# Optimization experiments

Hardware: AMD Instinct MI355X
Metric: run time of the kernel (lower is better)

## Reference

```python
import jax, jax.numpy as jnp
import numpy as np

D_MODEL = 96
N_HEAD = 3
HEAD_DIM = D_MODEL // N_HEAD  # 32
D_FF = 2048
WIDTH = 65
HALF_W = (WIDTH - 1) // 2  # 32
EPS = 1e-5


def layer_norm(x, g, b):
    mu = jnp.mean(x, axis=-1, keepdims=True)
    var = jnp.mean(jnp.square(x - mu), axis=-1, keepdims=True)
    return (x - mu) * jax.lax.rsqrt(var + EPS) * g + b


def setup_inputs() -> dict:
    key = jax.random.key(0)
    ks = jax.random.split(key, 8)
    B, T = 8, 2048
    s = 0.05
    return {
        "x": jax.random.normal(ks[0], (B, D_MODEL, T), dtype=jnp.float32),
        "w_qkv": jax.random.normal(ks[1], (3 * D_MODEL, D_MODEL), dtype=jnp.float32) * s,
        "b_qkv": jnp.zeros((3 * D_MODEL,), dtype=jnp.float32),
        "w_out": jax.random.normal(ks[2], (D_MODEL, D_MODEL), dtype=jnp.float32) * s,
        "b_out": jnp.zeros((D_MODEL,), dtype=jnp.float32),
        "ln1_g": jnp.ones((D_MODEL,), dtype=jnp.float32),
        "ln1_b": jnp.zeros((D_MODEL,), dtype=jnp.float32),
        "w_ff1": jax.random.normal(ks[3], (D_FF, D_MODEL), dtype=jnp.float32) * s,
        "b_ff1": jnp.zeros((D_FF,), dtype=jnp.float32),
        "w_ff2": jax.random.normal(ks[4], (D_MODEL, D_FF), dtype=jnp.float32) * s,
        "b_ff2": jnp.zeros((D_MODEL,), dtype=jnp.float32),
        "ln2_g": jnp.ones((D_MODEL,), dtype=jnp.float32),
        "ln2_b": jnp.zeros((D_MODEL,), dtype=jnp.float32),
        "lnf_g": jnp.ones((D_MODEL,), dtype=jnp.float32),
        "lnf_b": jnp.zeros((D_MODEL,), dtype=jnp.float32),
    }


def reference(x, w_qkv, b_qkv, w_out, b_out, ln1_g, ln1_b, w_ff1, b_ff1,
              w_ff2, b_ff2, ln2_g, ln2_b, lnf_g, lnf_b):
    # x: (B, C, T) -> (B, T, C)
    h = jnp.transpose(x, (0, 2, 1))
    B, T, C = h.shape

    # --- multi-head self-attention with banded mask ---
    qkv = h @ w_qkv.T + b_qkv                      # (B, T, 3C)
    q, k, v = jnp.split(qkv, 3, axis=-1)
    q = q.reshape(B, T, N_HEAD, HEAD_DIM)
    k = k.reshape(B, T, N_HEAD, HEAD_DIM)
    v = v.reshape(B, T, N_HEAD, HEAD_DIM)

    scale = 1.0 / jnp.sqrt(jnp.float32(HEAD_DIM))
    scores = jnp.einsum("bthd,bshd->bhts", q, k) * scale  # (B, H, T, T)

    idx = jnp.arange(T)
    band = jnp.abs(idx[:, None] - idx[None, :]) <= HALF_W  # |i-j| <= half width
    scores = jnp.where(band[None, None], scores, jnp.float32(-jnp.inf))

    attn = jax.nn.softmax(scores, axis=-1)
    ctx = jnp.einsum("bhts,bshd->bthd", attn, v).reshape(B, T, C)
    attn_out = ctx @ w_out.T + b_out

    # --- post-norm encoder layer (dropout inactive / eval mode) ---
    h = layer_norm(h + attn_out, ln1_g, ln1_b)
    ff = jax.nn.relu(h @ w_ff1.T + b_ff1) @ w_ff2.T + b_ff2
    h = layer_norm(h + ff, ln2_g, ln2_b)

    # extra layernorm applied when width is not None
    h = layer_norm(h, lnf_g, lnf_b)

    # (B, T, C) -> (B, C, T)
    return jnp.transpose(h, (0, 2, 1))
```

## Files before the change

kernel.cpp:

```cpp
#include <hip/hip_runtime.h>
#include <hip/hip_bf16.h>

#define B 8
#define T 2048
#define C 96
#define NH 3
#define HD 32
#define FFD 2048
#define HALF_W 32
#define BT (B*T)

typedef __hip_bfloat16 bf16;
typedef __attribute__((ext_vector_type(8))) short short8;
typedef __attribute__((ext_vector_type(4))) short short4v;
typedef __attribute__((ext_vector_type(16))) float floatx16;

__device__ __forceinline__ short f2bs(float v){
    __hip_bfloat16 h = __float2bfloat16(v);
    return *reinterpret_cast<short*>(&h);
}
__device__ __forceinline__ int imin(int a, int b){ return a < b ? a : b; }
__device__ __forceinline__ int imax(int a, int b){ return a > b ? a : b; }
__device__ __forceinline__ short8 ld_b64x2(const short* p){
    short4v a = *(const short4v*)p;
    short4v b = *(const short4v*)(p + 4);
    short8 v;
    v[0]=a[0]; v[1]=a[1]; v[2]=a[2]; v[3]=a[3];
    v[4]=b[0]; v[5]=b[1]; v[6]=b[2]; v[7]=b[3];
    return v;
}

__global__ void cvtw_kernel(const float* __restrict__ wq, const float* __restrict__ wo,
                            const float* __restrict__ w1, const float* __restrict__ w2,
                            bf16* __restrict__ dst){
    int i = blockIdx.x*256 + threadIdx.x;
    if(i < 27648)       dst[i] = __float2bfloat16(wq[i]);
    else if(i < 36864)  dst[i] = __float2bfloat16(wo[i-27648]);
    else if(i < 233472) dst[i] = __float2bfloat16(w1[i-36864]);
    else if(i < 430080) dst[i] = __float2bfloat16(w2[i-233472]);
}

__global__ __launch_bounds__(256) void qkv_kernel(
    const float* __restrict__ x, const bf16* __restrict__ wq,
    const float* __restrict__ bias, bf16* __restrict__ qkvs){
    __shared__ float xs[96*36];
    int b  = blockIdx.x >> 6;
    int t0 = (blockIdx.x & 63) * 32;
    for(int e = threadIdx.x; e < 96*8; e += 256){
        int c = e >> 3, t4 = e & 7;
        *(float4*)(xs + c*36 + t4*4) =
            *(const float4*)(x + (size_t)b*C*T + (size_t)c*T + t0 + t4*4);
    }
    __syncthreads();
    int r0 = b*T + t0;
    const int w = threadIdx.x >> 6, lane = threadIdx.x & 63;
    const int lm = lane & 31, hq = lane >> 5;
    short8 bfr[6];
    #pragma unroll
    for(int ks = 0; ks < 6; ++ks){
        short8 v;
        #pragma unroll
        for(int i = 0; i < 8; ++i)
            v[i] = f2bs(xs[(ks*16 + hq*8 + i)*36 + lm]);
        bfr[ks] = v;
    }
    int nacc = (w == 0) ? 3 : 2;
    int ots[3] = {w, w+4, 8};
    floatx16 acc[3];
    #pragma unroll
    for(int i = 0; i < 3; ++i)
        #pragma unroll
        for(int r = 0; r < 16; ++r) acc[i][r] = 0.f;
    #pragma unroll
    for(int i = 0; i < 3; ++i){
        if(i < nacc){
            #pragma unroll
            for(int ks = 0; ks < 6; ++ks){
                short8 af = *(const short8*)((const short*)wq
                              + (size_t)(ots[i]*32 + lm)*96 + ks*16 + hq*8);
                acc[i] = __builtin_amdgcn_mfma_f32_32x32x16_bf16(af, bfr[ks], acc[i], 0,0,0);
            }
        }
    }
    #pragma unroll
    for(int i = 0; i < 3; ++i){
        if(i < nacc){
            int type = ots[i]/3, hh = ots[i]%3;
            size_t rowbase = (((size_t)type*B*NH) + (size_t)b*NH + hh)*T + t0 + lm;
            #pragma unroll
            for(int q = 0; q < 4; ++q){
                float4 bv = *(const float4*)(bias + ots[i]*32 + 8*q + 4*hq);
                short4v pk;
                pk[0] = f2bs(acc[i][4*q+0] + bv.x);
                pk[1] = f2bs(acc[i][4*q+1] + bv.y);
                pk[2] = f2bs(acc[i][4*q+2] + bv.z);
                pk[3] = f2bs(acc[i][4*q+3] + bv.w);
                *(short4v*)((short*)qkvs + rowbase*32 + 8*q + 4*hq) = pk;
            }
        }
    }
}

__global__ __launch_bounds__(128) void attn_kernel(const bf16* __restrict__ qkvs,
                                                   bf16* __restrict__ ctxh){
    __shared__ __align__(16) short VtS[32*132];
    __shared__ __align__(16) short PtS[2][32*100];
    __shared__ float LsS[2][32];
    int blk = blockIdx.x;
    int ntile = T/64;
    int b   = blk / (NH*ntile);
    int rem = blk % (NH*ntile);
    int h   = rem / ntile;
    int t0  = (rem % ntile) * 64;
    const short* qb = (const short*)qkvs + ((size_t)0*B*NH + (size_t)b*NH + h)*T*32;
    const short* kb = (const short*)qkvs + ((size_t)1*B*NH + (size_t)b*NH + h)*T*32;
    const short* vb = (const short*)qkvs + ((size_t)2*B*NH + (size_t)b*NH + h)*T*32;
    const int tid = threadIdx.x;
    const int w = tid >> 6, lane = tid & 63;
    const int lm = lane & 31, hq = lane >> 5;

    for(int e = tid; e < 256; e += 128){
        int kp = e >> 2, d8 = e & 3;
        int sa = imin(imax(t0 - 32 + 2*kp, 0), T-1);
        int sb = imin(imax(t0 - 32 + 2*kp + 1, 0), T-1);
        short8 va = *(const short8*)(vb + (size_t)sa*32 + d8*8);
        short8 v2 = *(const short8*)(vb + (size_t)sb*32 + d8*8);
        #pragma unroll
        for(int j = 0; j < 8; ++j){
            int val = (int)(unsigned short)va[j] | ((int)(unsigned short)v2[j] << 16);
            *(int*)(VtS + (d8*8 + j)*132 + 2*kp) = val;
        }
    }
    short8 qf0, qf1;
    {
        const short* qrow = qb + (size_t)(t0 + 32*w + lm)*32;
        qf0 = *(const short8*)(qrow + hq*8);
        qf1 = *(const short8*)(qrow + 16 + hq*8);
    }
    floatx16 S[3];
    #pragma unroll
    for(int sub = 0; sub < 3; ++sub){
        int srow = imin(imax(t0 + 32*w - 32 + sub*32 + lm, 0), T-1);
        const short* krow = kb + (size_t)srow*32;
        short8 kf0 = *(const short8*)(krow + hq*8);
        short8 kf1 = *(const short8*)(krow + 16 + hq*8);
        floatx16 z;
        #pragma unroll
        for(int r = 0; r < 16; ++r) z[r] = 0.f;
        z = __builtin_amdgcn_mfma_f32_32x32x16_bf16(kf0, qf0, z, 0,0,0);
        z = __builtin_amdgcn_mfma_f32_32x32x16_bf16(kf1, qf1, z, 0,0,0);
        S[sub] = z;
    }
    const float scale = 0.17677669529663687f;
    float part = 0.f;
    #pragma unroll
    for(int sub = 0; sub < 3; ++sub){
        #pragma unroll
        for(int r = 0; r < 16; ++r){
            int key_local = sub*32 + (r&3) + 8*(r>>2) + 4*hq;
            int s_glob = t0 + 32*w - 32 + key_local;
            int rel = key_local - lm;
            bool ok = (rel >= 0) && (rel <= 64) && (s_glob >= 0) && (s_glob < T);
            float p = ok ? __expf(S[sub][r]*scale) : 0.f;
            S[sub][r] = p;
            part += p;
        }
    }
    float ltot = part + __shfl_xor(part, 32);
    if(hq == 0) LsS[w][lm] = ltot;
    #pragma unroll
    for(int sub = 0; sub < 3; ++sub){
        #pragma unroll
        for(int q4 = 0; q4 < 4; ++q4){
            int kbase = sub*32 + 8*q4 + 4*hq;
            short4v pk;
            pk[0] = f2bs(S[sub][4*q4+0]);
            pk[1] = f2bs(S[sub][4*q4+1]);
            pk[2] = f2bs(S[sub][4*q4+2]);
            pk[3] = f2bs(S[sub][4*q4+3]);
            *(short4v*)(PtS[w] + lm*100 + kbase) = pk;
        }
    }
    __syncthreads();
    floatx16 O;
    #pragma unroll
    for(int r = 0; r < 16; ++r) O[r] = 0.f;
    #pragma unroll
    for(int ks = 0; ks < 6; ++ks){
        short8 pa = ld_b64x2(PtS[w] + lm*100 + ks*16 + hq*8);
        short8 vf = ld_b64x2(VtS + lm*132 + 32*w + ks*16 + hq*8);
        O = __builtin_amdgcn_mfma_f32_32x32x16_bf16(pa, vf, O, 0,0,0);
    }
    #pragma unroll
    for(int r = 0; r < 16; ++r){
        int qr = (r&3) + 8*(r>>2) + 4*hq;
        float linv = 1.f / LsS[w][qr];
        ((short*)ctxh)[(((size_t)b*NH + h)*T + t0 + 32*w + qr)*32 + lm] = f2bs(O[r]*linv);
    }
}

__global__ __launch_bounds__(192) void outproj_ln_kernel(
    const bf16* __restrict__ ctxh, const bf16* __restrict__ wo,
    const float* __restrict__ bias, const float* __restrict__ x,
    const float* __restrict__ g1, const float* __restrict__ bb1,
    float* __restrict__ h1, bf16* __restrict__ h1b){
    __shared__ float red[2][3][32];
    const int ct = threadIdx.x >> 6, lane = threadIdx.x & 63;
    const int lm = lane & 31, hq = lane >> 5;
    const int r0 = blockIdx.x * 32;
    const int b = r0 / T, tloc = r0 % T;
    short8 bfr[6];
    #pragma unroll
    for(int ks = 0; ks < 6; ++ks){
        int off = ks*16 + hq*8;
        int hh = off >> 5, dd = off & 31;
        bfr[ks] = *(const short8*)((const short*)ctxh
                    + (((size_t)b*NH + hh)*T + tloc + lm)*32 + dd);
    }
    floatx16 acc;
    #pragma unroll
    for(int r = 0; r < 16; ++r) acc[r] = 0.f;
    #pragma unroll
    for(int ks = 0; ks < 6; ++ks){
        short8 af = *(const short8*)((const short*)wo
                      + (size_t)(ct*32 + lm)*96 + ks*16 + hq*8);
        acc = __builtin_amdgcn_mfma_f32_32x32x16_bf16(af, bfr[ks], acc, 0,0,0);
    }
    float vals[16];
    float p1 = 0.f, p2 = 0.f;
    #pragma unroll
    for(int q = 0; q < 4; ++q){
        int c = ct*32 + 8*q + 4*hq;
        float4 bv = *(const float4*)(bias + c);
        float bva[4] = {bv.x, bv.y, bv.z, bv.w};
        #pragma unroll
        for(int r = 0; r < 4; ++r){
            float xv = x[(size_t)b*C*T + (size_t)(c + r)*T + tloc + lm];
            float v = acc[4*q+r] + bva[r] + xv;
            vals[4*q+r] = v;
            p1 += v; p2 += v*v;
        }
    }
    p1 += __shfl_xor(p1, 32);
    p2 += __shfl_xor(p2, 32);
    if(hq == 0){ red[0][ct][lm] = p1; red[1][ct][lm] = p2; }
    __syncthreads();
    float s  = red[0][0][lm] + red[0][1][lm] + red[0][2][lm];
    float s2 = red[1][0][lm] + red[1][1][lm] + red[1][2][lm];
    float mu = s * (1.0f/96.0f);
    float rstd = rsqrtf(s2*(1.0f/96.0f) - mu*mu + 1e-5f);
    int row = r0 + lm;
    #pragma unroll
    for(int q = 0; q < 4; ++q){
        int c = ct*32 + 8*q + 4*hq;
        float4 gv = *(const float4*)(g1 + c);
        float4 bv = *(const float4*)(bb1 + c);
        float ga[4] = {gv.x, gv.y, gv.z, gv.w};
        float ba[4] = {bv.x, bv.y, bv.z, bv.w};
        float4 yo;
        float ya[4];
        #pragma unroll
        for(int r = 0; r < 4; ++r)
            ya[r] = (vals[4*q+r] - mu)*rstd*ga[r] + ba[r];
        yo.x = ya[0]; yo.y = ya[1]; yo.z = ya[2]; yo.w = ya[3];
        *(float4*)(h1 + (size_t)row*96 + c) = yo;
        short4v pk;
        #pragma unroll
        for(int r = 0; r < 4; ++r) pk[r] = f2bs(ya[r]);
        *(short4v*)((short*)h1b + (size_t)row*96 + c) = pk;
    }
}

__global__ __launch_bounds__(256) void ff_ln_kernel(
    const bf16* __restrict__ h1b, const float* __restrict__ h1,
    const bf16* __restrict__ w1b, const float* __restrict__ b1,
    const bf16* __restrict__ w2b, const float* __restrict__ b2,
    const float* __restrict__ g2, const float* __restrict__ bt2,
    const float* __restrict__ gf, const float* __restrict__ btf,
    float* __restrict__ out){
    __shared__ __align__(16) short sst[32*132];
    __shared__ float redp[9*1088];
    __shared__ float zt[96*33];
    const int tid = threadIdx.x;
    const int w = tid >> 6, lane = tid & 63;
    const int lm = lane & 31, hq = lane >> 5;
    const int r0 = blockIdx.x * 32;
    short8 hf[6];
    #pragma unroll
    for(int ks = 0; ks < 6; ++ks)
        hf[ks] = *(const short8*)((const short*)h1b
                   + (size_t)(r0 + lm)*96 + ks*16 + hq*8);
    floatx16 acc2[3];
    #pragma unroll
    for(int i = 0; i < 3; ++i)
        #pragma unroll
        for(int r = 0; r < 16; ++r) acc2[i][r] = 0.f;
    for(int jt = 0; jt < 16; ++jt){
        const int j0 = jt * 128;
        floatx16 a0;
        #pragma unroll
        for(int r = 0; r < 16; ++r) a0[r] = 0.f;
        #pragma unroll
        for(int ks = 0; ks < 6; ++ks){
            short8 af = *(const short8*)((const short*)w1b
                          + (size_t)(j0 + w*32 + lm)*96 + ks*16 + hq*8);
            a0 = __builtin_amdgcn_mfma_f32_32x32x16_bf16(af, hf[ks], a0, 0,0,0);
        }
        #pragma unroll
        for(int q = 0; q < 4; ++q){
            float4 bv = *(const float4*)(b1 + j0 + w*32 + 8*q + 4*hq);
            float bva[4] = {bv.x, bv.y, bv.z, bv.w};
            short4v pk;
            #pragma unroll
            for(int r = 0; r < 4; ++r){
                float v = a0[4*q+r] + bva[r];
                pk[r] = f2bs(v > 0.f ? v : 0.f);
            }
            *(short4v*)(sst + lm*132 + w*32 + 8*q + 4*hq) = pk;
        }
        #pragma unroll
        for(int g = 0; g < 2; ++g){
            int jl0 = w*32 + g*16;
            short8 sf = ld_b64x2(sst + lm*132 + jl0 + hq*8);
            #pragma unroll
            for(int ct = 0; ct < 3; ++ct){
                short8 wf = *(const short8*)((const short*)w2b
                              + (size_t)(ct*32 + lm)*FFD + j0 + jl0 + hq*8);
                acc2[ct] = __builtin_amdgcn_mfma_f32_32x32x16_bf16(wf, sf, acc2[ct], 0,0,0);
            }
        }
    }
    __syncthreads();
    if(w > 0){
        #pragma unroll
        for(int ct = 0; ct < 3; ++ct)
            #pragma unroll
            for(int q = 0; q < 4; ++q)
                #pragma unroll
                for(int r = 0; r < 4; ++r)
                    redp[((w-1)*3 + ct)*1088 + lane*17 + 4*q + r] = acc2[ct][4*q+r];
    }
    __syncthreads();
    if(w == 0){
        float vals[48];
        float p1 = 0.f, p2 = 0.f;
        #pragma unroll
        for(int ct = 0; ct < 3; ++ct){
            #pragma unroll
            for(int q = 0; q < 4; ++q){
                int c = ct*32 + 8*q + 4*hq;
                float4 bv = *(const float4*)(b2 + c);
                float4 rs = *(const float4*)(h1 + (size_t)(r0 + lm)*96 + c);
                float bva[4] = {bv.x, bv.y, bv.z, bv.w};
                float rsa[4] = {rs.x, rs.y, rs.z, rs.w};
                #pragma unroll
                for(int r = 0; r < 4; ++r){
                    float v = acc2[ct][4*q+r]
                            + redp[(0*3 + ct)*1088 + lane*17 + 4*q + r]
                            + redp[(1*3 + ct)*1088 + lane*17 + 4*q + r]
                            + redp[(2*3 + ct)*1088 + lane*17 + 4*q + r]
                            + bva[r] + rsa[r];
                    vals[ct*16 + 4*q + r] = v;
                    p1 += v; p2 += v*v;
                }
            }
        }
        p1 += __shfl_xor(p1, 32);
        p2 += __shfl_xor(p2, 32);
        float mu = p1*(1.0f/96.0f);
        float rstd = rsqrtf(p2*(1.0f/96.0f) - mu*mu + 1e-5f);
        float q1 = 0.f, q2 = 0.f;
        #pragma unroll
        for(int ct = 0; ct < 3; ++ct){
            #pragma unroll
            for(int q = 0; q < 4; ++q){
                int c = ct*32 + 8*q + 4*hq;
                float4 gv = *(const float4*)(g2 + c);
                float4 bv = *(const float4*)(bt2 + c);
                float ga[4] = {gv.x, gv.y, gv.z, gv.w};
                float ba[4] = {bv.x, bv.y, bv.z, bv.w};
                #pragma unroll
                for(int r = 0; r < 4; ++r){
                    float y = (vals[ct*16+4*q+r] - mu)*rstd*ga[r] + ba[r];
                    vals[ct*16+4*q+r] = y;
                    q1 += y; q2 += y*y;
                }
            }
        }
        q1 += __shfl_xor(q1, 32);
        q2 += __shfl_xor(q2, 32);
        float mu2 = q1*(1.0f/96.0f);
        float rstd2 = rsqrtf(q2*(1.0f/96.0f) - mu2*mu2 + 1e-5f);
        #pragma unroll
        for(int ct = 0; ct < 3; ++ct){
            #pragma unroll
            for(int q = 0; q < 4; ++q){
                int c = ct*32 + 8*q + 4*hq;
                float4 gv = *(const float4*)(gf + c);
                float4 bv = *(const float4*)(btf + c);
                float ga[4] = {gv.x, gv.y, gv.z, gv.w};
                float ba[4] = {bv.x, bv.y, bv.z, bv.w};
                #pragma unroll
                for(int r = 0; r < 4; ++r)
                    zt[(c + r)*33 + lm] = (vals[ct*16+4*q+r] - mu2)*rstd2*ga[r] + ba[r];
            }
        }
    }
    __syncthreads();
    int bb  = r0 / T;
    int t0g = r0 % T;
    for(int e = tid; e < 96*32; e += 256){
        int c = e >> 5, tt = e & 31;
        out[(size_t)bb*C*T + (size_t)c*T + t0g + tt] = zt[c*33 + tt];
    }
}

extern "C" void kernel_launch(void* const* d_in, const int* in_sizes, int n_in,
                              void* d_out, int out_size, void* d_ws, size_t ws_size,
                              hipStream_t stream) {
    const float* x     = (const float*)d_in[0];
    const float* w_qkv = (const float*)d_in[1];
    const float* b_qkv = (const float*)d_in[2];
    const float* w_out = (const float*)d_in[3];
    const float* b_out = (const float*)d_in[4];
    const float* ln1_g = (const float*)d_in[5];
    const float* ln1_b = (const float*)d_in[6];
    const float* w_ff1 = (const float*)d_in[7];
    const float* b_ff1 = (const float*)d_in[8];
    const float* w_ff2 = (const float*)d_in[9];
    const float* b_ff2 = (const float*)d_in[10];
    const float* ln2_g = (const float*)d_in[11];
    const float* ln2_b = (const float*)d_in[12];
    const float* lnf_g = (const float*)d_in[13];
    const float* lnf_b = (const float*)d_in[14];
    float* out = (float*)d_out;

    char* wsb = (char*)d_ws;
    bf16*  qkvs  = (bf16*)wsb;
    bf16*  ctxh  = (bf16*)(wsb + 9437184);
    float* h1    = (float*)(wsb + 12582912);
    bf16*  h1b   = (bf16*)(wsb + 18874368);
    bf16*  wts   = (bf16*)(wsb + 22020096);
    bf16*  wqkvb = wts;
    bf16*  woutb = wts + 27648;
    bf16*  w1b   = wts + 36864;
    bf16*  w2b   = wts + 233472;

    cvtw_kernel      <<<1680, 256, 0, stream>>>(w_qkv, w_out, w_ff1, w_ff2, wts);
    qkv_kernel       <<<BT/32, 256, 0, stream>>>(x, wqkvb, b_qkv, qkvs);
    attn_kernel      <<<B*NH*(T/64), 128, 0, stream>>>(qkvs, ctxh);
    outproj_ln_kernel<<<BT/32, 192, 0, stream>>>(ctxh, woutb, b_out, x,
                                                 ln1_g, ln1_b, h1, h1b);
    ff_ln_kernel     <<<BT/32, 256, 0, stream>>>(h1b, h1, w1b, b_ff1, w2b, b_ff2,
                                                 ln2_g, ln2_b, lnf_g, lnf_b, out);
}
```

Baseline: 151.8 us.

## Prefetch FF weights, split MFMA chains, and pass FF1 output via lane shuffles

Restructures the FF inner loop. W1 fragments for the next tile are prefetched into registers, and the W2 fragments are loaded at the start of each iteration. The FF1 MFMA chain is split into two independent accumulators to shorten the dependency chain. The shared-memory staging of the ReLU output is replaced with cross-half-wave shuffles, and the loop is fully unrolled with occupancy hinted at two blocks. This targets global-load latency and LDS round trips, at the cost of higher register pressure, which may cause spills under the new launch bound.

```diff
diff --git a/kernel.cpp b/kernel.cpp
--- a/kernel.cpp
+++ b/kernel.cpp
@@ -271,14 +271,13 @@
     }
 }
 
-__global__ __launch_bounds__(256) void ff_ln_kernel(
+__global__ __launch_bounds__(256, 2) void ff_ln_kernel(
     const bf16* __restrict__ h1b, const float* __restrict__ h1,
     const bf16* __restrict__ w1b, const float* __restrict__ b1,
     const bf16* __restrict__ w2b, const float* __restrict__ b2,
     const float* __restrict__ g2, const float* __restrict__ bt2,
     const float* __restrict__ gf, const float* __restrict__ btf,
     float* __restrict__ out){
-    __shared__ __align__(16) short sst[32*132];
     __shared__ float redp[9*1088];
     __shared__ float zt[96*33];
     const int tid = threadIdx.x;
@@ -295,40 +294,67 @@
     for(int i = 0; i < 3; ++i)
         #pragma unroll
         for(int r = 0; r < 16; ++r) acc2[i][r] = 0.f;
+
+    const short* w1p = (const short*)w1b + (size_t)(w*32 + lm)*96 + hq*8;
+    const short* w2p = (const short*)w2b + hq*8;
+    short8 cw1[6];
+    #pragma unroll
+    for(int ks = 0; ks < 6; ++ks)
+        cw1[ks] = *(const short8*)(w1p + ks*16);
+
+    #pragma unroll
     for(int jt = 0; jt < 16; ++jt){
-        const int j0 = jt * 128;
-        floatx16 a0;
-        #pragma unroll
-        for(int r = 0; r < 16; ++r) a0[r] = 0.f;
-        #pragma unroll
-        for(int ks = 0; ks < 6; ++ks){
-            short8 af = *(const short8*)((const short*)w1b
-                          + (size_t)(j0 + w*32 + lm)*96 + ks*16 + hq*8);
-            a0 = __builtin_amdgcn_mfma_f32_32x32x16_bf16(af, hf[ks], a0, 0,0,0);
-        }
+        const int jn = (jt + 1) & 15;
+        short8 nw1[6], w2f[6];
+        #pragma unroll
+        for(int ks = 0; ks < 6; ++ks)
+            nw1[ks] = *(const short8*)(w1p + (size_t)jn*128*96 + ks*16);
+        #pragma unroll
+        for(int g = 0; g < 2; ++g)
+            #pragma unroll
+            for(int ct = 0; ct < 3; ++ct)
+                w2f[g*3 + ct] = *(const short8*)(w2p
+                                  + (size_t)(ct*32 + lm)*FFD + jt*128 + w*32 + g*16);
+        floatx16 aA, aB;
+        #pragma unroll
+        for(int r = 0; r < 16; ++r){ aA[r] = 0.f; aB[r] = 0.f; }
+        #pragma unroll
+        for(int ks = 0; ks < 3; ++ks){
+            aA = __builtin_amdgcn_mfma_f32_32x32x16_bf16(cw1[2*ks],   hf[2*ks],   aA, 0,0,0);
+            aB = __builtin_amdgcn_mfma_f32_32x32x16_bf16(cw1[2*ks+1], hf[2*ks+1], aB, 0,0,0);
+        }
+        int pk[4][2];
         #pragma unroll
         for(int q = 0; q < 4; ++q){
-            float4 bv = *(const float4*)(b1 + j0 + w*32 + 8*q + 4*hq);
+            float4 bv = *(const float4*)(b1 + jt*128 + w*32 + 8*q + 4*hq);
             float bva[4] = {bv.x, bv.y, bv.z, bv.w};
-            short4v pk;
+            short4v t;
             #pragma unroll
             for(int r = 0; r < 4; ++r){
-                float v = a0[4*q+r] + bva[r];
-                pk[r] = f2bs(v > 0.f ? v : 0.f);
-            }
-            *(short4v*)(sst + lm*132 + w*32 + 8*q + 4*hq) = pk;
+                float v = aA[4*q+r] + aB[4*q+r] + bva[r];
+                t[r] = f2bs(v > 0.f ? v : 0.f);
+            }
+            int2 u = *(int2*)&t;
+            pk[q][0] = u.x; pk[q][1] = u.y;
         }
         #pragma unroll
         for(int g = 0; g < 2; ++g){
-            int jl0 = w*32 + g*16;
-            short8 sf = ld_b64x2(sst + lm*132 + jl0 + hq*8);
-            #pragma unroll
-            for(int ct = 0; ct < 3; ++ct){
-                short8 wf = *(const short8*)((const short*)w2b
-                              + (size_t)(ct*32 + lm)*FFD + j0 + jl0 + hq*8);
-                acc2[ct] = __builtin_amdgcn_mfma_f32_32x32x16_bf16(wf, sf, acc2[ct], 0,0,0);
-            }
-        }
+            int a0 = pk[2*g][0],   a1 = pk[2*g][1];
+            int b0 = pk[2*g+1][0], b1v = pk[2*g+1][1];
+            int ra0 = __shfl_xor(a0, 32),  ra1 = __shfl_xor(a1, 32);
+            int rb0 = __shfl_xor(b0, 32),  rb1 = __shfl_xor(b1v, 32);
+            int4 sfi;
+            sfi.x = hq ? rb0 : a0;
+            sfi.y = hq ? rb1 : a1;
+            sfi.z = hq ? b0  : ra0;
+            sfi.w = hq ? b1v : ra1;
+            short8 sf = *(short8*)&sfi;
+            #pragma unroll
+            for(int ct = 0; ct < 3; ++ct)
+                acc2[ct] = __builtin_amdgcn_mfma_f32_32x32x16_bf16(w2f[g*3+ct], sf, acc2[ct], 0,0,0);
+        }
+        #pragma unroll
+        for(int ks = 0; ks < 6; ++ks) cw1[ks] = nw1[ks];
     }
     __syncthreads();
     if(w > 0){
```

After: 155.3 us. 1.02x slower.
